# Kernel optimization log

Measured on AMD Instinct MI355X. Metric: run time of the kernel, lower is better.

## Reference

```python
import jax, jax.numpy as jnp
import numpy as np

N, E, F_IN = 50000, 250000, 128
H1, H2, HEADS = 64, 32, 4
D1 = H1 * HEADS   # 256 = conv1 output dim (concat)
D2 = H2 * HEADS   # 128 = conv2 output dim (concat)
EPS_BN = 1e-5


def setup_inputs() -> dict:
    key = jax.random.key(0)
    ks = iter(jax.random.split(key, 64))
    def nrm(shape, scale=0.05):
        return jax.random.normal(next(ks), shape, dtype=jnp.float32) * scale
    inp = {}
    inp['x'] = jax.random.normal(next(ks), (N, F_IN), dtype=jnp.float32)
    inp['edge_index'] = jax.random.randint(next(ks), (2, E), 0, N, dtype=jnp.int32)
    inp['neg_edge_index'] = jax.random.randint(next(ks), (2, E), 0, N, dtype=jnp.int32)
    # conv1: TransformerConv(F_IN, 64, heads=4, beta=True, concat=True)
    inp['Wq1'] = nrm((F_IN, D1)); inp['bq1'] = jnp.zeros((D1,), jnp.float32)
    inp['Wk1'] = nrm((F_IN, D1)); inp['bk1'] = jnp.zeros((D1,), jnp.float32)
    inp['Wv1'] = nrm((F_IN, D1)); inp['bv1'] = jnp.zeros((D1,), jnp.float32)
    inp['Ws1'] = nrm((F_IN, D1)); inp['bs1'] = jnp.zeros((D1,), jnp.float32)
    inp['Wb1'] = nrm((3 * D1, 1))
    inp['g1'] = jnp.ones((D1,), jnp.float32); inp['be1'] = jnp.zeros((D1,), jnp.float32)
    inp['m1'] = nrm((D1,), 0.01); inp['v1'] = jax.random.uniform(next(ks), (D1,), dtype=jnp.float32) + 0.5
    # conv2: TransformerConv(256, 32, heads=4, beta=True, concat=True)
    inp['Wq2'] = nrm((D1, D2)); inp['bq2'] = jnp.zeros((D2,), jnp.float32)
    inp['Wk2'] = nrm((D1, D2)); inp['bk2'] = jnp.zeros((D2,), jnp.float32)
    inp['Wv2'] = nrm((D1, D2)); inp['bv2'] = jnp.zeros((D2,), jnp.float32)
    inp['Ws2'] = nrm((D1, D2)); inp['bs2'] = jnp.zeros((D2,), jnp.float32)
    inp['Wb2'] = nrm((3 * D2, 1))
    inp['g2'] = jnp.ones((D2,), jnp.float32); inp['be2'] = jnp.zeros((D2,), jnp.float32)
    inp['m2'] = nrm((D2,), 0.01); inp['v2'] = jax.random.uniform(next(ks), (D2,), dtype=jnp.float32) + 0.5
    # conv3: TransformerConv(128, 1, heads=1, beta=True, concat=False)
    inp['Wq3'] = nrm((D2, 1)); inp['bq3'] = jnp.zeros((1,), jnp.float32)
    inp['Wk3'] = nrm((D2, 1)); inp['bk3'] = jnp.zeros((1,), jnp.float32)
    inp['Wv3'] = nrm((D2, 1)); inp['bv3'] = jnp.zeros((1,), jnp.float32)
    inp['Ws3'] = nrm((D2, 1)); inp['bs3'] = jnp.zeros((1,), jnp.float32)
    inp['Wb3'] = nrm((3, 1))
    inp['c1'] = jnp.float32(0.5); inp['c2'] = jnp.float32(0.5)
    return inp


def _tconv(h, src, dst, Wq, bq, Wk, bk, Wv, bv, Ws, bs, Wb, heads, dh):
    # PyG TransformerConv with beta=True, root_weight=True. Messages flow src -> dst.
    n = h.shape[0]
    q = (h @ Wq + bq).reshape(n, heads, dh)
    k = (h @ Wk + bk).reshape(n, heads, dh)
    v = (h @ Wv + bv).reshape(n, heads, dh)
    score = jnp.einsum('ehd,ehd->eh', q[dst], k[src]) / jnp.sqrt(jnp.float32(dh))  # [E,H]
    m = jax.ops.segment_max(score, dst, num_segments=n)
    m = jnp.where(jnp.isfinite(m), m, jnp.float32(0.0))  # empty segments
    p = jnp.exp(score - m[dst])
    denom = jax.ops.segment_sum(p, dst, num_segments=n)
    alpha = p / (denom[dst] + 1e-16)
    out = jax.ops.segment_sum(alpha[:, :, None] * v[src], dst, num_segments=n)  # [N,H,dh]
    out = out.reshape(n, heads * dh)  # concat (heads=1 for conv3 -> same as mean)
    x_r = h @ Ws + bs
    beta = jax.nn.sigmoid(jnp.concatenate([out, x_r, out - x_r], axis=-1) @ Wb)  # [N,1]
    return beta * x_r + (1.0 - beta) * out


def _bn_eval(x, g, b, m, v):
    return (x - m) * jax.lax.rsqrt(v + EPS_BN) * g + b


def reference(x, edge_index, neg_edge_index,
              Wq1, bq1, Wk1, bk1, Wv1, bv1, Ws1, bs1, Wb1, g1, be1, m1, v1,
              Wq2, bq2, Wk2, bk2, Wv2, bv2, Ws2, bs2, Wb2, g2, be2, m2, v2,
              Wq3, bq3, Wk3, bk3, Wv3, bv3, Ws3, bs3, Wb3, c1, c2):
    src, dst = edge_index[0], edge_index[1]
    h = _tconv(x, src, dst, Wq1, bq1, Wk1, bk1, Wv1, bv1, Ws1, bs1, Wb1, HEADS, H1)
    h = jax.nn.elu(_bn_eval(h, g1, be1, m1, v1))
    h = _tconv(h, src, dst, Wq2, bq2, Wk2, bk2, Wv2, bv2, Ws2, bs2, Wb2, HEADS, H2)
    z = jax.nn.elu(_bn_eval(h, g2, be2, m2, v2))
    pos = -jnp.log(jax.nn.sigmoid(jnp.sum(z[src] * z[dst], axis=1)) + 1e-15).mean()
    ns, nd = neg_edge_index[0], neg_edge_index[1]
    neg = -jnp.log(1.0 - jax.nn.sigmoid(jnp.sum(z[ns] * z[nd], axis=1)) + 1e-15).mean()
    r_loss = pos + neg
    x_out = _tconv(z, src, dst, Wq3, bq3, Wk3, bk3, Wv3, bv3, Ws3, bs3, Wb3, 1, 1)
    return (x_out, r_loss, c1, c2)
```

## Files before the change

### kernel.cpp

```cpp
#include <hip/hip_runtime.h>
#include <hip/hip_bf16.h>

typedef _Float16 half8 __attribute__((ext_vector_type(8)));
typedef float f32x4 __attribute__((ext_vector_type(4)));

__global__ __launch_bounds__(256) void prep_w(
    const float* __restrict__ W0, const float* __restrict__ W1,
    const float* __restrict__ W2, const float* __restrict__ W3,
    _Float16* __restrict__ T, int K, int D)
{
  int idx = blockIdx.x * 256 + threadIdx.x;
  int tot = K * D;
  if (idx >= 4 * tot) return;
  int which = idx / tot, rem = idx - which * tot;
  int d = rem / K, k = rem - d * K;
  const float* W = which == 0 ? W0 : which == 1 ? W1 : which == 2 ? W2 : W3;
  T[idx] = (_Float16)W[(long long)k * D + d];
}

template<int K>
__global__ __launch_bounds__(256) void mfma_gemm(
    const float* __restrict__ A, const _Float16* __restrict__ Wt,
    const float* __restrict__ bias, float* __restrict__ C, int Nr, int Dout)
{
  int lane = threadIdx.x & 63;
  int w    = threadIdx.x >> 6;
  int wm = w >> 1, wn = w & 1;
  int row0 = blockIdx.x * 64 + wm * 32;
  int col0 = blockIdx.y * 64 + wn * 32;
  int lr = lane & 15;
  int lk = (lane >> 4) * 8;

  f32x4 acc[2][2] = {};
#pragma unroll
  for (int kb = 0; kb < K; kb += 32) {
    half8 a[2], b[2];
#pragma unroll
    for (int mt = 0; mt < 2; ++mt) {
      int row = row0 + mt * 16 + lr;
      if (row < Nr) {
        const float* p = A + (long long)row * K + kb + lk;
        float4 f0 = *(const float4*)p;
        float4 f1 = *(const float4*)(p + 4);
        a[mt][0] = (_Float16)f0.x; a[mt][1] = (_Float16)f0.y;
        a[mt][2] = (_Float16)f0.z; a[mt][3] = (_Float16)f0.w;
        a[mt][4] = (_Float16)f1.x; a[mt][5] = (_Float16)f1.y;
        a[mt][6] = (_Float16)f1.z; a[mt][7] = (_Float16)f1.w;
      } else {
        a[mt] = half8{};
      }
    }
#pragma unroll
    for (int nt = 0; nt < 2; ++nt) {
      int col = col0 + nt * 16 + lr;
      b[nt] = *(const half8*)(Wt + (long long)col * K + kb + lk);
    }
#pragma unroll
    for (int mt = 0; mt < 2; ++mt)
#pragma unroll
      for (int nt = 0; nt < 2; ++nt)
        acc[mt][nt] = __builtin_amdgcn_mfma_f32_16x16x32_f16(a[mt], b[nt], acc[mt][nt], 0, 0, 0);
  }
#pragma unroll
  for (int nt = 0; nt < 2; ++nt) {
    int col = col0 + nt * 16 + lr;
    float bc = bias[col];
#pragma unroll
    for (int mt = 0; mt < 2; ++mt) {
      int r0 = row0 + mt * 16 + (lane >> 4) * 4;
#pragma unroll
      for (int i = 0; i < 4; ++i) {
        int row = r0 + i;
        if (row < Nr) C[(long long)row * Dout + col] = acc[mt][nt][i] + bc;
      }
    }
  }
}

__global__ __launch_bounds__(256) void csr_hist(
    const int* __restrict__ ei, int E, int* __restrict__ cnt)
{
  int e = blockIdx.x * 256 + threadIdx.x;
  if (e >= E) return;
  atomicAdd(&cnt[ei[E + e]], 1);
}

__global__ __launch_bounds__(256) void csr_scan1(
    const int* __restrict__ cnt, int* __restrict__ excl,
    int* __restrict__ chunkSums, int N)
{
  int b = blockIdx.x, t = threadIdx.x;
  int lane = t & 63, w = t >> 6;
  int base = b * 1024 + t * 4;
  int c[4];
#pragma unroll
  for (int j = 0; j < 4; ++j) c[j] = (base + j < N) ? cnt[base + j] : 0;
  int ts = c[0] + c[1] + c[2] + c[3];
  int s = ts;
#pragma unroll
  for (int d = 1; d < 64; d <<= 1) {
    int u = __shfl_up(s, d, 64);
    if (lane >= d) s += u;
  }
  __shared__ int wsum[4];
  if (lane == 63) wsum[w] = s;
  __syncthreads();
  int woff = 0;
  for (int i = 0; i < w; ++i) woff += wsum[i];
  int off = woff + s - ts;
#pragma unroll
  for (int j = 0; j < 4; ++j) {
    if (base + j < N) excl[base + j] = off;
    off += c[j];
  }
  if (t == 0) chunkSums[b] = wsum[0] + wsum[1] + wsum[2] + wsum[3];
}

__global__ void csr_scan2(int* __restrict__ chunkSums, int nch,
                          int* __restrict__ rowptr, int N, int E)
{
  int lane = threadIdx.x;
  int v = (lane < nch) ? chunkSums[lane] : 0;
  int s = v;
#pragma unroll
  for (int d = 1; d < 64; d <<= 1) {
    int u = __shfl_up(s, d, 64);
    if (lane >= d) s += u;
  }
  if (lane < nch) chunkSums[lane] = s - v;
  if (lane == 0) rowptr[N] = E;
}

__global__ __launch_bounds__(256) void csr_scan3(
    int* __restrict__ rowptr, const int* __restrict__ chunkSums, int N)
{
  int i = blockIdx.x * 256 + threadIdx.x;
  if (i < N) rowptr[i] += chunkSums[i >> 10];
}

__global__ __launch_bounds__(256) void csr_scatter(
    const int* __restrict__ ei, int E, const int* __restrict__ rowptr,
    int* __restrict__ fill, int* __restrict__ csr_src)
{
  int e = blockIdx.x * 256 + threadIdx.x;
  if (e >= E) return;
  int s = ei[e], d = ei[E + e];
  int pos = atomicAdd(&fill[d], 1);
  csr_src[rowptr[d] + pos] = s;
}

template<int D, int H>
__global__ __launch_bounds__(256) void attn_fused(
    const int* __restrict__ rowptr, const int* __restrict__ csr_src,
    const float* __restrict__ q, const float* __restrict__ k,
    const float* __restrict__ v, float* __restrict__ o, int N)
{
  constexpr int PER = D / 64;
  constexpr int DH  = D / H;
  int node = blockIdx.x * 4 + (threadIdx.x >> 6);
  if (node >= N) return;
  int lane = threadIdx.x & 63;
  int j0   = lane * PER;
  const float inv = 1.0f / sqrtf((float)DH);

  float qv[PER];
  if constexpr (PER == 4) {
    float4 t4 = *(const float4*)(q + (long long)node * D + j0);
    qv[0]=t4.x; qv[1]=t4.y; qv[2]=t4.z; qv[3]=t4.w;
  } else {
    float2 t2 = *(const float2*)(q + (long long)node * D + j0);
    qv[0]=t2.x; qv[1]=t2.y;
  }

  float m = -INFINITY, den = 0.f;
  float acc[PER] = {};
  int beg = rowptr[node], end = rowptr[node + 1];
  for (int i = beg; i < end; ++i) {
    int s = csr_src[i];
    float kv[PER], vv[PER];
    if constexpr (PER == 4) {
      float4 t4 = *(const float4*)(k + (long long)s * D + j0);
      kv[0]=t4.x; kv[1]=t4.y; kv[2]=t4.z; kv[3]=t4.w;
      float4 u4 = *(const float4*)(v + (long long)s * D + j0);
      vv[0]=u4.x; vv[1]=u4.y; vv[2]=u4.z; vv[3]=u4.w;
    } else {
      float2 t2 = *(const float2*)(k + (long long)s * D + j0);
      kv[0]=t2.x; kv[1]=t2.y;
      float2 u2 = *(const float2*)(v + (long long)s * D + j0);
      vv[0]=u2.x; vv[1]=u2.y;
    }
    float dot = 0.f;
#pragma unroll
    for (int j = 0; j < PER; ++j) dot += qv[j] * kv[j];
    dot += __shfl_xor(dot, 8, 64);
    dot += __shfl_xor(dot, 4, 64);
    dot += __shfl_xor(dot, 2, 64);
    dot += __shfl_xor(dot, 1, 64);
    float score = dot * inv;
    float nm = fmaxf(m, score);
    float scale = __expf(m - nm);
    float p = __expf(score - nm);
    den = den * scale + p;
#pragma unroll
    for (int j = 0; j < PER; ++j) acc[j] = acc[j] * scale + p * vv[j];
    m = nm;
  }
  float r = 1.f / (den + 1e-16f);
  if constexpr (PER == 4) {
    float4 w4; w4.x = acc[0]*r; w4.y = acc[1]*r; w4.z = acc[2]*r; w4.w = acc[3]*r;
    *(float4*)(o + (long long)node * D + j0) = w4;
  } else {
    float2 w2; w2.x = acc[0]*r; w2.y = acc[1]*r;
    *(float2*)(o + (long long)node * D + j0) = w2;
  }
}

template<int D>
__global__ __launch_bounds__(256) void node_gate2(
    const float* __restrict__ o, const float* __restrict__ xr,
    const float* __restrict__ Wb, const float* __restrict__ g,
    const float* __restrict__ be, const float* __restrict__ bm,
    const float* __restrict__ bv, float* __restrict__ out, int N)
{
  constexpr int PER = D / 64;
  int node = blockIdx.x * 4 + (threadIdx.x >> 6);
  if (node >= N) return;
  int lane = threadIdx.x & 63;
  int j0   = lane * PER;
  float ov[PER], xv[PER];
  if constexpr (PER == 4) {
    float4 o4 = *(const float4*)(o  + (long long)node * D + j0);
    float4 x4 = *(const float4*)(xr + (long long)node * D + j0);
    ov[0]=o4.x; ov[1]=o4.y; ov[2]=o4.z; ov[3]=o4.w;
    xv[0]=x4.x; xv[1]=x4.y; xv[2]=x4.z; xv[3]=x4.w;
  } else {
    float2 o2 = *(const float2*)(o  + (long long)node * D + j0);
    float2 x2 = *(const float2*)(xr + (long long)node * D + j0);
    ov[0]=o2.x; ov[1]=o2.y;
    xv[0]=x2.x; xv[1]=x2.y;
  }
  float dot = 0.f;
#pragma unroll
  for (int i = 0; i < PER; ++i) {
    int j = j0 + i;
    dot += ov[i] * Wb[j] + xv[i] * Wb[D + j] + (ov[i] - xv[i]) * Wb[2 * D + j];
  }
#pragma unroll
  for (int off = 32; off >= 1; off >>= 1) dot += __shfl_xor(dot, off, 64);
  float beta = 1.f / (1.f + expf(-dot));
  float res[PER];
#pragma unroll
  for (int i = 0; i < PER; ++i) {
    int j = j0 + i;
    float h = beta * xv[i] + (1.f - beta) * ov[i];
    float y = (h - bm[j]) * rsqrtf(bv[j] + 1e-5f) * g[j] + be[j];
    res[i] = y > 0.f ? y : expf(y) - 1.f;
  }
  if constexpr (PER == 4) {
    float4 w; w.x=res[0]; w.y=res[1]; w.z=res[2]; w.w=res[3];
    *(float4*)(out + (long long)node * D + j0) = w;
  } else {
    float2 w; w.x=res[0]; w.y=res[1];
    *(float2*)(out + (long long)node * D + j0) = w;
  }
}

__global__ __launch_bounds__(256) void loss_kernel(
    const int* __restrict__ ei, const int* __restrict__ nei,
    const float* __restrict__ z, int E, float* __restrict__ acc)
{
  int lane = threadIdx.x & 63;
  int wib  = threadIdx.x >> 6;
  int sub  = lane >> 5, r = lane & 31;
  long long gw = ((long long)blockIdx.x * blockDim.x + threadIdx.x) >> 6;
  long long nw = ((long long)gridDim.x * blockDim.x) >> 6;
  float lpos = 0.f, lneg = 0.f;
  for (long long w = gw * 2 + sub; w < 2LL * E; w += nw * 2) {
    int isneg = (w >= E);
    const int* ep = isneg ? nei : ei;
    long long idx = isneg ? w - E : w;
    int s = ep[idx], d = ep[E + idx];
    float4 a = *(const float4*)(z + (long long)s * 128 + r * 4);
    float4 b = *(const float4*)(z + (long long)d * 128 + r * 4);
    float dot = a.x * b.x + a.y * b.y + a.z * b.z + a.w * b.w;
#pragma unroll
    for (int off = 16; off >= 1; off >>= 1) dot += __shfl_xor(dot, off, 64);
    if (r == 0) {
      float sg = 1.f / (1.f + expf(-dot));
      if (isneg) lneg += -logf(1.f - sg + 1e-15f);
      else       lpos += -logf(sg + 1e-15f);
    }
  }
#pragma unroll
  for (int off = 32; off >= 1; off >>= 1) {
    lpos += __shfl_xor(lpos, off, 64);
    lneg += __shfl_xor(lneg, off, 64);
  }
  __shared__ float sp[4], sn[4];
  if (lane == 0) { sp[wib] = lpos; sn[wib] = lneg; }
  __syncthreads();
  if (threadIdx.x == 0) {
    float P = 0.f, Ng = 0.f;
    for (int i = 0; i < 4; ++i) { P += sp[i]; Ng += sn[i]; }
    atomicAdd(acc, P);
    atomicAdd(acc + 1, Ng);
  }
}

__global__ __launch_bounds__(256) void gemv4(
    const float* __restrict__ z,
    const float* __restrict__ Wq, const float* __restrict__ bq,
    const float* __restrict__ Wk, const float* __restrict__ bk,
    const float* __restrict__ Wv, const float* __restrict__ bv,
    const float* __restrict__ Ws, const float* __restrict__ bs,
    float* __restrict__ q3, float* __restrict__ k3,
    float* __restrict__ v3, float* __restrict__ s3, int N)
{
  int node = blockIdx.x * 4 + (threadIdx.x >> 6);
  if (node >= N) return;
  int lane = threadIdx.x & 63;
  float2 zv = *(const float2*)(z + (long long)node * 128 + lane * 2);
  float aq = zv.x * Wq[lane*2] + zv.y * Wq[lane*2+1];
  float ak = zv.x * Wk[lane*2] + zv.y * Wk[lane*2+1];
  float av = zv.x * Wv[lane*2] + zv.y * Wv[lane*2+1];
  float as_ = zv.x * Ws[lane*2] + zv.y * Ws[lane*2+1];
#pragma unroll
  for (int off = 32; off >= 1; off >>= 1) {
    aq  += __shfl_xor(aq,  off, 64);
    ak  += __shfl_xor(ak,  off, 64);
    av  += __shfl_xor(av,  off, 64);
    as_ += __shfl_xor(as_, off, 64);
  }
  if (lane == 0) {
    q3[node] = aq + bq[0];
    k3[node] = ak + bk[0];
    v3[node] = av + bv[0];
    s3[node] = as_ + bs[0];
  }
}

__global__ __launch_bounds__(256) void attn3_node(
    const int* __restrict__ rowptr, const int* __restrict__ csr_src,
    const float* __restrict__ q3, const float* __restrict__ k3,
    const float* __restrict__ v3, const float* __restrict__ s3,
    const float* __restrict__ Wb3, float* __restrict__ out, int N)
{
  int n = blockIdx.x * 256 + threadIdx.x;
  if (n >= N) return;
  float qd = q3[n];
  float m = -INFINITY, den = 0.f, acc = 0.f;
  int beg = rowptr[n], end = rowptr[n + 1];
  for (int i = beg; i < end; ++i) {
    int s = csr_src[i];
    float sc = qd * k3[s];
    float nm = fmaxf(m, sc);
    float scale = __expf(m - nm);
    float p = __expf(sc - nm);
    den = den * scale + p;
    acc = acc * scale + p * v3[s];
    m = nm;
  }
  float on = acc / (den + 1e-16f);
  float xr = s3[n];
  float tv = on * Wb3[0] + xr * Wb3[1] + (on - xr) * Wb3[2];
  float b = 1.f / (1.f + expf(-tv));
  out[n] = b * xr + (1.f - b) * on;
}

__global__ void finalize_kernel(const float* __restrict__ acc,
                                const float* __restrict__ c1, const float* __restrict__ c2,
                                float* __restrict__ out, int N, int E)
{
  out[N]     = acc[0] / (float)E + acc[1] / (float)E;
  out[N + 1] = c1[0];
  out[N + 2] = c2[0];
}

extern "C" void kernel_launch(void* const* d_in, const int* in_sizes, int n_in,
                              void* d_out, int out_size, void* d_ws, size_t ws_size,
                              hipStream_t stream)
{
  const float* x   = (const float*)d_in[0];
  const int*   ei  = (const int*)d_in[1];
  const int*   nei = (const int*)d_in[2];
  const float* Wq1 = (const float*)d_in[3];  const float* bq1 = (const float*)d_in[4];
  const float* Wk1 = (const float*)d_in[5];  const float* bk1 = (const float*)d_in[6];
  const float* Wv1 = (const float*)d_in[7];  const float* bv1 = (const float*)d_in[8];
  const float* Ws1 = (const float*)d_in[9];  const float* bs1 = (const float*)d_in[10];
  const float* Wb1 = (const float*)d_in[11];
  const float* g1  = (const float*)d_in[12]; const float* be1 = (const float*)d_in[13];
  const float* m1  = (const float*)d_in[14]; const float* v1  = (const float*)d_in[15];
  const float* Wq2 = (const float*)d_in[16]; const float* bq2 = (const float*)d_in[17];
  const float* Wk2 = (const float*)d_in[18]; const float* bk2 = (const float*)d_in[19];
  const float* Wv2 = (const float*)d_in[20]; const float* bv2 = (const float*)d_in[21];
  const float* Ws2 = (const float*)d_in[22]; const float* bs2 = (const float*)d_in[23];
  const float* Wb2 = (const float*)d_in[24];
  const float* g2  = (const float*)d_in[25]; const float* be2 = (const float*)d_in[26];
  const float* m2  = (const float*)d_in[27]; const float* v2  = (const float*)d_in[28];
  const float* Wq3 = (const float*)d_in[29]; const float* bq3 = (const float*)d_in[30];
  const float* Wk3 = (const float*)d_in[31]; const float* bk3 = (const float*)d_in[32];
  const float* Wv3 = (const float*)d_in[33]; const float* bv3 = (const float*)d_in[34];
  const float* Ws3 = (const float*)d_in[35]; const float* bs3 = (const float*)d_in[36];
  const float* Wb3 = (const float*)d_in[37];
  const float* c1  = (const float*)d_in[38]; const float* c2  = (const float*)d_in[39];

  const int N = in_sizes[0] / 128;
  const int E = in_sizes[1] / 2;

  float* ws = (float*)d_ws;
  float* B0 = ws;
  float* B1 = B0 + (size_t)N * 256;
  float* B2 = B1 + (size_t)N * 256;
  int* rowptr = (int*)(B2 + (size_t)N * 256);
  int* cnt    = rowptr + (N + 1);
  int* csrs   = cnt + N;
  int* chks   = csrs + E;
  float* accbuf = (float*)(chks + 64);
  uintptr_t wp = ((uintptr_t)(accbuf + 2) + 63) & ~(uintptr_t)63;
  _Float16* wt1 = (_Float16*)wp;
  _Float16* wt2 = wt1 + 4 * 32768;

  size_t need = ((size_t)3 * N * 256) * 4 + ((size_t)2 * N + 1 + E + 64) * 4 + 8
              + 64 + 8 * 32768 * sizeof(_Float16);
  if (ws_size < need) return;

  float* out = (float*)d_out;
  dim3 blk(256);
  int ng  = (N + 3) / 4;
  int egE = (E + 255) / 256;
  int egN = (N + 255) / 256;
  int nch = (N + 1023) / 1024;
  dim3 g1grid((N + 63) / 64, 256 / 64);
  dim3 g2grid((N + 63) / 64, 128 / 64);

  prep_w<<<(4 * 32768 + 255) / 256, blk, 0, stream>>>(Wq1, Wk1, Wv1, Ws1, wt1, 128, 256);
  prep_w<<<(4 * 32768 + 255) / 256, blk, 0, stream>>>(Wq2, Wk2, Wv2, Ws2, wt2, 256, 128);

  (void)hipMemsetAsync(cnt, 0, (size_t)N * sizeof(int), stream);
  csr_hist<<<egE, blk, 0, stream>>>(ei, E, cnt);
  csr_scan1<<<nch, blk, 0, stream>>>(cnt, rowptr, chks, N);
  csr_scan2<<<1, 64, 0, stream>>>(chks, nch, rowptr, N, E);
  csr_scan3<<<egN, blk, 0, stream>>>(rowptr, chks, N);
  (void)hipMemsetAsync(cnt, 0, (size_t)N * sizeof(int), stream);
  csr_scatter<<<egE, blk, 0, stream>>>(ei, E, rowptr, cnt, csrs);

  mfma_gemm<128><<<g1grid, blk, 0, stream>>>(x, wt1 + 0 * 32768, bq1, B0, N, 256);
  mfma_gemm<128><<<g1grid, blk, 0, stream>>>(x, wt1 + 1 * 32768, bk1, B1, N, 256);
  mfma_gemm<128><<<g1grid, blk, 0, stream>>>(x, wt1 + 2 * 32768, bv1, B2, N, 256);
  attn_fused<256,4><<<ng, blk, 0, stream>>>(rowptr, csrs, B0, B1, B2, B0, N);
  mfma_gemm<128><<<g1grid, blk, 0, stream>>>(x, wt1 + 3 * 32768, bs1, B1, N, 256);
  node_gate2<256><<<ng, blk, 0, stream>>>(B0, B1, Wb1, g1, be1, m1, v1, B2, N);

  float* q2p = B0;
  float* k2p = B0 + (size_t)N * 128;
  float* v2p = B1;
  float* s2p = B1 + (size_t)N * 128;
  mfma_gemm<256><<<g2grid, blk, 0, stream>>>(B2, wt2 + 0 * 32768, bq2, q2p, N, 128);
  mfma_gemm<256><<<g2grid, blk, 0, stream>>>(B2, wt2 + 1 * 32768, bk2, k2p, N, 128);
  mfma_gemm<256><<<g2grid, blk, 0, stream>>>(B2, wt2 + 2 * 32768, bv2, v2p, N, 128);
  attn_fused<128,4><<<ng, blk, 0, stream>>>(rowptr, csrs, q2p, k2p, v2p, q2p, N);
  mfma_gemm<256><<<g2grid, blk, 0, stream>>>(B2, wt2 + 3 * 32768, bs2, s2p, N, 128);
  float* z = k2p;
  node_gate2<128><<<ng, blk, 0, stream>>>(q2p, s2p, Wb2, g2, be2, m2, v2, z, N);

  (void)hipMemsetAsync(accbuf, 0, 2 * sizeof(float), stream);
  loss_kernel<<<1024, blk, 0, stream>>>(ei, nei, z, E, accbuf);

  float* q3 = B1;
  float* k3 = B1 + (size_t)N;
  float* v3 = B1 + (size_t)2 * N;
  float* s3 = B1 + (size_t)3 * N;
  gemv4<<<ng, blk, 0, stream>>>(z, Wq3, bq3, Wk3, bk3, Wv3, bv3, Ws3, bs3, q3, k3, v3, s3, N);
  attn3_node<<<egN, blk, 0, stream>>>(rowptr, csrs, q3, k3, v3, s3, Wb3, out, N);

  finalize_kernel<<<1, 1, 0, stream>>>(accbuf, c1, c2, out, N, E);
}
```

Baseline: 852.3 us.

## Store K/V projections and loss embeddings in fp16 to halve gather traffic

The K and V projection GEMMs now write fp16 outputs, and the attention kernels gather those half-precision rows, converting them to fp32 for the math. The second node-gate kernel also emits an fp16 copy of z, which the loss kernel gathers in place of the fp32 z. The loss grid is doubled. This targets the bandwidth of the random per-edge gathers, at the cost of fp16 rounding in scores, aggregated values and the loss dot products.

```diff
diff --git a/kernel.cpp b/kernel.cpp
--- a/kernel.cpp
+++ b/kernel.cpp
@@ -2,6 +2,8 @@
 #include <hip/hip_bf16.h>
 
 typedef _Float16 half8 __attribute__((ext_vector_type(8)));
+typedef _Float16 half4 __attribute__((ext_vector_type(4)));
+typedef _Float16 half2v __attribute__((ext_vector_type(2)));
 typedef float f32x4 __attribute__((ext_vector_type(4)));
 
 __global__ __launch_bounds__(256) void prep_w(
@@ -18,10 +20,10 @@
   T[idx] = (_Float16)W[(long long)k * D + d];
 }
 
-template<int K>
+template<int K, typename OutT>
 __global__ __launch_bounds__(256) void mfma_gemm(
     const float* __restrict__ A, const _Float16* __restrict__ Wt,
-    const float* __restrict__ bias, float* __restrict__ C, int Nr, int Dout)
+    const float* __restrict__ bias, OutT* __restrict__ C, int Nr, int Dout)
 {
   int lane = threadIdx.x & 63;
   int w    = threadIdx.x >> 6;
@@ -71,7 +73,7 @@
 #pragma unroll
       for (int i = 0; i < 4; ++i) {
         int row = r0 + i;
-        if (row < Nr) C[(long long)row * Dout + col] = acc[mt][nt][i] + bc;
+        if (row < Nr) C[(long long)row * Dout + col] = (OutT)(acc[mt][nt][i] + bc);
       }
     }
   }
@@ -152,8 +154,8 @@
 template<int D, int H>
 __global__ __launch_bounds__(256) void attn_fused(
     const int* __restrict__ rowptr, const int* __restrict__ csr_src,
-    const float* __restrict__ q, const float* __restrict__ k,
-    const float* __restrict__ v, float* __restrict__ o, int N)
+    const float* __restrict__ q, const _Float16* __restrict__ k,
+    const _Float16* __restrict__ v, float* __restrict__ o, int N)
 {
   constexpr int PER = D / 64;
   constexpr int DH  = D / H;
@@ -179,15 +181,15 @@
     int s = csr_src[i];
     float kv[PER], vv[PER];
     if constexpr (PER == 4) {
-      float4 t4 = *(const float4*)(k + (long long)s * D + j0);
-      kv[0]=t4.x; kv[1]=t4.y; kv[2]=t4.z; kv[3]=t4.w;
-      float4 u4 = *(const float4*)(v + (long long)s * D + j0);
-      vv[0]=u4.x; vv[1]=u4.y; vv[2]=u4.z; vv[3]=u4.w;
+      half4 t4 = *(const half4*)(k + (long long)s * D + j0);
+      half4 u4 = *(const half4*)(v + (long long)s * D + j0);
+#pragma unroll
+      for (int j = 0; j < 4; ++j) { kv[j] = (float)t4[j]; vv[j] = (float)u4[j]; }
     } else {
-      float2 t2 = *(const float2*)(k + (long long)s * D + j0);
-      kv[0]=t2.x; kv[1]=t2.y;
-      float2 u2 = *(const float2*)(v + (long long)s * D + j0);
-      vv[0]=u2.x; vv[1]=u2.y;
+      half2v t2 = *(const half2v*)(k + (long long)s * D + j0);
+      half2v u2 = *(const half2v*)(v + (long long)s * D + j0);
+#pragma unroll
+      for (int j = 0; j < 2; ++j) { kv[j] = (float)t2[j]; vv[j] = (float)u2[j]; }
     }
     float dot = 0.f;
 #pragma unroll
@@ -215,12 +217,13 @@
   }
 }
 
-template<int D>
+template<int D, bool WRITE_H>
 __global__ __launch_bounds__(256) void node_gate2(
     const float* __restrict__ o, const float* __restrict__ xr,
     const float* __restrict__ Wb, const float* __restrict__ g,
     const float* __restrict__ be, const float* __restrict__ bm,
-    const float* __restrict__ bv, float* __restrict__ out, int N)
+    const float* __restrict__ bv, float* __restrict__ out,
+    _Float16* __restrict__ outh, int N)
 {
   constexpr int PER = D / 64;
   int node = blockIdx.x * 4 + (threadIdx.x >> 6);
@@ -263,11 +266,21 @@
     float2 w; w.x=res[0]; w.y=res[1];
     *(float2*)(out + (long long)node * D + j0) = w;
   }
+  if constexpr (WRITE_H) {
+    if constexpr (PER == 4) {
+      half4 hw; hw[0]=(_Float16)res[0]; hw[1]=(_Float16)res[1];
+      hw[2]=(_Float16)res[2]; hw[3]=(_Float16)res[3];
+      *(half4*)(outh + (long long)node * D + j0) = hw;
+    } else {
+      half2v hw; hw[0]=(_Float16)res[0]; hw[1]=(_Float16)res[1];
+      *(half2v*)(outh + (long long)node * D + j0) = hw;
+    }
+  }
 }
 
 __global__ __launch_bounds__(256) void loss_kernel(
     const int* __restrict__ ei, const int* __restrict__ nei,
-    const float* __restrict__ z, int E, float* __restrict__ acc)
+    const _Float16* __restrict__ zh, int E, float* __restrict__ acc)
 {
   int lane = threadIdx.x & 63;
   int wib  = threadIdx.x >> 6;
@@ -280,9 +293,10 @@
     const int* ep = isneg ? nei : ei;
     long long idx = isneg ? w - E : w;
     int s = ep[idx], d = ep[E + idx];
-    float4 a = *(const float4*)(z + (long long)s * 128 + r * 4);
-    float4 b = *(const float4*)(z + (long long)d * 128 + r * 4);
-    float dot = a.x * b.x + a.y * b.y + a.z * b.z + a.w * b.w;
+    half4 a = *(const half4*)(zh + (long long)s * 128 + r * 4);
+    half4 b = *(const half4*)(zh + (long long)d * 128 + r * 4);
+    float dot = (float)a[0]*(float)b[0] + (float)a[1]*(float)b[1]
+              + (float)a[2]*(float)b[2] + (float)a[3]*(float)b[3];
 #pragma unroll
     for (int off = 16; off >= 1; off >>= 1) dot += __shfl_xor(dot, off, 64);
     if (r == 0) {
@@ -444,27 +458,30 @@
   (void)hipMemsetAsync(cnt, 0, (size_t)N * sizeof(int), stream);
   csr_scatter<<<egE, blk, 0, stream>>>(ei, E, rowptr, cnt, csrs);
 
-  mfma_gemm<128><<<g1grid, blk, 0, stream>>>(x, wt1 + 0 * 32768, bq1, B0, N, 256);
-  mfma_gemm<128><<<g1grid, blk, 0, stream>>>(x, wt1 + 1 * 32768, bk1, B1, N, 256);
-  mfma_gemm<128><<<g1grid, blk, 0, stream>>>(x, wt1 + 2 * 32768, bv1, B2, N, 256);
-  attn_fused<256,4><<<ng, blk, 0, stream>>>(rowptr, csrs, B0, B1, B2, B0, N);
-  mfma_gemm<128><<<g1grid, blk, 0, stream>>>(x, wt1 + 3 * 32768, bs1, B1, N, 256);
-  node_gate2<256><<<ng, blk, 0, stream>>>(B0, B1, Wb1, g1, be1, m1, v1, B2, N);
-
-  float* q2p = B0;
-  float* k2p = B0 + (size_t)N * 128;
-  float* v2p = B1;
-  float* s2p = B1 + (size_t)N * 128;
-  mfma_gemm<256><<<g2grid, blk, 0, stream>>>(B2, wt2 + 0 * 32768, bq2, q2p, N, 128);
-  mfma_gemm<256><<<g2grid, blk, 0, stream>>>(B2, wt2 + 1 * 32768, bk2, k2p, N, 128);
-  mfma_gemm<256><<<g2grid, blk, 0, stream>>>(B2, wt2 + 2 * 32768, bv2, v2p, N, 128);
-  attn_fused<128,4><<<ng, blk, 0, stream>>>(rowptr, csrs, q2p, k2p, v2p, q2p, N);
-  mfma_gemm<256><<<g2grid, blk, 0, stream>>>(B2, wt2 + 3 * 32768, bs2, s2p, N, 128);
-  float* z = k2p;
-  node_gate2<128><<<ng, blk, 0, stream>>>(q2p, s2p, Wb2, g2, be2, m2, v2, z, N);
+  _Float16* k1h = (_Float16*)B1;
+  _Float16* v1h = (_Float16*)B2;
+  mfma_gemm<128, float>   <<<g1grid, blk, 0, stream>>>(x, wt1 + 0 * 32768, bq1, B0,  N, 256);
+  mfma_gemm<128, _Float16><<<g1grid, blk, 0, stream>>>(x, wt1 + 1 * 32768, bk1, k1h, N, 256);
+  mfma_gemm<128, _Float16><<<g1grid, blk, 0, stream>>>(x, wt1 + 2 * 32768, bv1, v1h, N, 256);
+  attn_fused<256,4><<<ng, blk, 0, stream>>>(rowptr, csrs, B0, k1h, v1h, B0, N);
+  mfma_gemm<128, float>   <<<g1grid, blk, 0, stream>>>(x, wt1 + 3 * 32768, bs1, B1, N, 256);
+  node_gate2<256,false><<<ng, blk, 0, stream>>>(B0, B1, Wb1, g1, be1, m1, v1, B2, nullptr, N);
+
+  float*    q2p = B0;
+  _Float16* k2h = (_Float16*)(B0 + (size_t)N * 128);
+  _Float16* v2h = (_Float16*)B1;
+  float*    s2p = B1 + (size_t)N * 128;
+  mfma_gemm<256, float>   <<<g2grid, blk, 0, stream>>>(B2, wt2 + 0 * 32768, bq2, q2p, N, 128);
+  mfma_gemm<256, _Float16><<<g2grid, blk, 0, stream>>>(B2, wt2 + 1 * 32768, bk2, k2h, N, 128);
+  mfma_gemm<256, _Float16><<<g2grid, blk, 0, stream>>>(B2, wt2 + 2 * 32768, bv2, v2h, N, 128);
+  attn_fused<128,4><<<ng, blk, 0, stream>>>(rowptr, csrs, q2p, k2h, v2h, q2p, N);
+  mfma_gemm<256, float>   <<<g2grid, blk, 0, stream>>>(B2, wt2 + 3 * 32768, bs2, s2p, N, 128);
+  float*    z  = B0 + (size_t)N * 128;
+  _Float16* zh = (_Float16*)B2;
+  node_gate2<128,true><<<ng, blk, 0, stream>>>(q2p, s2p, Wb2, g2, be2, m2, v2, z, zh, N);
 
   (void)hipMemsetAsync(accbuf, 0, 2 * sizeof(float), stream);
-  loss_kernel<<<1024, blk, 0, stream>>>(ei, nei, z, E, accbuf);
+  loss_kernel<<<2048, blk, 0, stream>>>(ei, nei, zh, E, accbuf);
 
   float* q3 = B1;
   float* k3 = B1 + (size_t)N;
```

Result: faster. 798.8 us (-6.3%).
